# Performance work log

Hardware: AMD Instinct MI355X
Metric: run time of the kernel (lower is better)

Reference implementation:

```python
import jax, jax.numpy as jnp
import numpy as np

L, S = 3, 5                 # A hierarchy layers, subsets per layer
CIN = COUT = 64
INTER = COUT // (S - 1)     # 16
BC = COUT // 4              # 16 channels per TCN branch
N, T, V = 128, 128, 25
KS = 5
DILS = (1, 2)
EPS = 1e-5


def setup_inputs() -> dict:
    key = jax.random.key(0)
    ks = jax.random.split(key, 22)
    rn = lambda i, shape, s=0.1: jax.random.normal(ks[i], shape, jnp.float32) * s
    g1 = lambda i, shape: 1.0 + jax.random.normal(ks[i], shape, jnp.float32) * 0.05
    return {
        'x':      jax.random.normal(ks[0], (N, CIN, T, V), jnp.float32),
        'PA':     rn(1, (L, S, V, V), 0.2),
        'gdw':    rn(2, (L, INTER, CIN)),
        'gdb':    rn(3, (L, INTER)),
        'gdg':    g1(4, (L, INTER)),
        'gdbt':   rn(5, (L, INTER)),
        'gsw':    rn(6, (L, S, INTER, INTER)),
        'gsb':    rn(7, (L, S, INTER)),
        'gsg':    g1(8, (L, S, INTER)),
        'gsbt':   rn(9, (L, S, INTER)),
        'gbng':   g1(10, (COUT,)),
        'gbnb':   rn(11, (COUT,)),
        'brw':    rn(12, (4, BC, COUT)),
        'brb':    rn(13, (4, BC)),
        'brg':    g1(14, (4, BC)),
        'brbt':   rn(15, (4, BC)),
        'tcw':    rn(16, (2, BC, BC, KS, 1)),
        'tcbias': rn(17, (2, BC)),
        'tcg':    g1(18, (2, BC)),
        'tcbt':   rn(19, (2, BC)),
        'mpg':    g1(20, (BC,)),
        'mpb':    rn(21, (BC,)),
    }


def _bn(x, g, b):
    # training-mode BatchNorm2d over (N, T, V) with biased variance
    m = x.mean(axis=(0, 2, 3), keepdims=True)
    v = ((x - m) ** 2).mean(axis=(0, 2, 3), keepdims=True)
    return (x - m) * jax.lax.rsqrt(v + EPS) * g[None, :, None, None] + b[None, :, None, None]


def _c1x1(x, w, b=None):
    y = jnp.einsum('nctv,oc->notv', x, w)
    return y if b is None else y + b[None, :, None, None]


def reference(x, PA, gdw, gdb, gdg, gdbt, gsw, gsb, gsg, gsbt, gbng, gbnb,
              brw, brb, brg, brbt, tcw, tcbias, tcg, tcbt, mpg, mpb):
    # ---- UbH_Gconv ----
    layer_outs = []
    for i in range(L):
        xd = jax.nn.relu(_bn(_c1x1(x, gdw[i], gdb[i]), gdg[i], gdbt[i]))
        ys = [
            _bn(_c1x1(jnp.einsum('nctu,vu->nctv', xd, PA[i, j]), gsw[i, j], gsb[i, j]),
                gsg[i, j], gsbt[i, j])
            for j in range(S)
        ]
        layer_outs.append(jnp.concatenate(ys, axis=1))      # [N, S*INTER, T, V]
    out = jnp.stack(layer_outs, axis=2)                     # [N, S*INTER, L, T, V]
    base = out[:, :INTER]                                   # subset-0 block
    new = out[:, INTER:] + jnp.tile(base, (1, S - 1, 1, 1, 1))
    new = new.sum(axis=2)                                   # sum over hierarchy layers -> [N, COUT, T, V]
    xg = jax.nn.relu(_bn(new, gbng, gbnb) + x)              # residual down is identity (CIN==COUT)

    # ---- MultiScale_TemporalConv (residual=False) ----
    branches = []
    for k, d in enumerate(DILS):
        y = jax.nn.relu(_bn(_c1x1(xg, brw[k], brb[k]), brg[k], brbt[k]))
        pad = (KS + (KS - 1) * (d - 1) - 1) // 2
        y = jax.lax.conv_general_dilated(
            y, tcw[k], window_strides=(1, 1), padding=((pad, pad), (0, 0)),
            rhs_dilation=(d, 1), dimension_numbers=('NCHW', 'OIHW', 'NCHW'))
        y = y + tcbias[k][None, :, None, None]
        branches.append(_bn(y, tcg[k], tcbt[k]))
    # maxpool branch
    y = jax.nn.relu(_bn(_c1x1(xg, brw[2], brb[2]), brg[2], brbt[2]))
    y = jax.lax.reduce_window(y, -jnp.inf, jax.lax.max, (1, 1, 3, 1), (1, 1, 1, 1),
                              ((0, 0), (0, 0), (1, 1), (0, 0)))
    branches.append(_bn(y, mpg, mpb))
    # plain 1x1 branch
    branches.append(_bn(_c1x1(xg, brw[3], brb[3]), brg[3], brbt[3]))

    t = jnp.concatenate(branches, axis=1)                   # [N, COUT, T, V]
    # unit residual is identity (CIN==COUT, stride==1)
    return jax.nn.relu(t + xg)
```

## Files before the change

### kernel.cpp

```cpp
#include <hip/hip_runtime.h>

#define N_ 128
#define T_ 128
#define V_ 25
#define TV 3200
#define LL 3
#define SS 5
#define II 16
#define EPSB 1e-5f
#define MCNT 409600.0f


__device__ __forceinline__ float2 bncoef(const float2* st, int slot, float g, float bt){
  float2 s = st[slot];
  float m  = s.x * (1.0f/MCNT);
  float var = s.y * (1.0f/MCNT) - m*m;
  float a = g * rsqrtf(var + EPSB);
  return make_float2(a, bt - m*a);
}

__global__ __launch_bounds__(256) void k1_conv_dw(
    const float* __restrict__ x, const float* __restrict__ gdw, const float* __restrict__ gdb,
    float* __restrict__ c1, float2* st)
{
  __shared__ float w[64*48];
  __shared__ float bias[48];
  __shared__ float bst[4][96];
  const int tid = threadIdx.x;
  for (int i = tid; i < 64*48; i += 256){ int c = i/48, o = i - c*48; w[i] = gdw[o*64 + c]; }
  if (tid < 48) bias[tid] = gdb[tid];
  __syncthreads();
  const int n = blockIdx.y;
  const int rem = blockIdx.x*256 + tid;
  const bool act = rem < TV;
  float acc[48];
  #pragma unroll
  for (int o = 0; o < 48; o++) acc[o] = act ? bias[o] : 0.f;
  const float* xp = x + (size_t)n*64*TV + rem;
  if (act){
    #pragma unroll 4
    for (int c = 0; c < 64; c++){
      float xv = xp[c*TV];
      const float4* w4 = (const float4*)&w[c*48];
      #pragma unroll
      for (int o4 = 0; o4 < 12; o4++){
        float4 ww = w4[o4];
        acc[o4*4+0] += ww.x*xv; acc[o4*4+1] += ww.y*xv;
        acc[o4*4+2] += ww.z*xv; acc[o4*4+3] += ww.w*xv;
      }
    }
    #pragma unroll
    for (int o = 0; o < 48; o++){
      int l = o >> 4, oi = o & 15;
      c1[(size_t)((l*N_+n)*II + oi)*TV + rem] = acc[o];
    }
  }
  const int wv = tid >> 6, lane = tid & 63;
  #pragma unroll
  for (int o = 0; o < 48; o++){
    float s = acc[o], q = acc[o]*acc[o];
    #pragma unroll
    for (int m = 32; m; m >>= 1){ s += __shfl_xor(s, m); q += __shfl_xor(q, m); }
    if (lane == 0){ bst[wv][2*o] = s; bst[wv][2*o+1] = q; }
  }
  __syncthreads();
  float* stf = (float*)st;
  if (tid < 96) unsafeAtomicAdd(stf + tid, bst[0][tid]+bst[1][tid]+bst[2][tid]+bst[3][tid]);
}

__global__ __launch_bounds__(256) void k2_spatial_stats(
    const float* __restrict__ c1, const float* __restrict__ PA,
    const float* __restrict__ gsw, const float* __restrict__ gsb,
    const float* __restrict__ gdg, const float* __restrict__ gdbt,
    float2* st)
{
  __shared__ float zz[4][25][16];
  __shared__ float bst[4][160];
  const int tid = threadIdx.x;
  const int l = blockIdx.z, n = blockIdx.y;
  const int wu = __builtin_amdgcn_readfirstlane(tid >> 6);
  const int lane = tid & 63;
  const int t2 = lane >> 4, oc = lane & 15;
  const int t = blockIdx.x*4 + t2;
  float cAr, cBr;
  {
    float2 s = st[l*16+oc];
    float m = s.x*(1.f/MCNT), var = s.y*(1.f/MCNT) - m*m;
    cAr = gdg[l*16+oc]*rsqrtf(var+EPSB);
    cBr = gdbt[l*16+oc] - m*cAr;
  }
  float xdr[25];
  {
    const float* c1p = c1 + ((size_t)((l*N_+n)*II + oc))*TV + t*25;
    #pragma unroll
    for (int u = 0; u < 25; u++) xdr[u] = fmaxf(cAr*c1p[u] + cBr, 0.f);
  }
  #pragma unroll 1
  for (int j = 0; j < 5; j++){
    const float* paJ = PA + (size_t)(l*5+j)*625;
    const float* gwp = gsw + ((size_t)((l*5+j)*16 + oc))*16;
    float gwr[16];
    #pragma unroll
    for (int c4 = 0; c4 < 4; c4++){
      float4 g4 = *(const float4*)(gwp + 4*c4);
      gwr[4*c4+0]=g4.x; gwr[4*c4+1]=g4.y; gwr[4*c4+2]=g4.z; gwr[4*c4+3]=g4.w;
    }
    const float bjo = gsb[(l*5+j)*16 + oc];
    float ssum = 0.f, sq = 0.f;
    #pragma unroll
    for (int i = 0; i < 7; i++){
      const int vreal = wu + 4*i;
      const int v = vreal < 25 ? vreal : 24;
      const float* par = paJ + v*25;
      float pan[25];
      #pragma unroll
      for (int u = 0; u < 25; u++) pan[u] = par[u];
      if (vreal < 25){
        float z0 = xdr[0]*pan[0], z1 = xdr[1]*pan[1], z2 = xdr[2]*pan[2], z3 = xdr[3]*pan[3];
        #pragma unroll
        for (int u = 4; u < 24; u += 4){
          z0 += xdr[u+0]*pan[u+0];
          z1 += xdr[u+1]*pan[u+1];
          z2 += xdr[u+2]*pan[u+2];
          z3 += xdr[u+3]*pan[u+3];
        }
        z0 += xdr[24]*pan[24];
        zz[t2][v][oc] = (z0+z1)+(z2+z3);
        const float4* zr = (const float4*)&zz[t2][v][0];
        float4 za = zr[0], zb = zr[1], zc = zr[2], zd = zr[3];
        float d0 = gwr[0]*za.x + gwr[1]*za.y + gwr[2]*za.z + gwr[3]*za.w;
        float d1 = gwr[4]*zb.x + gwr[5]*zb.y + gwr[6]*zb.z + gwr[7]*zb.w;
        float d2 = gwr[8]*zc.x + gwr[9]*zc.y + gwr[10]*zc.z + gwr[11]*zc.w;
        float d3 = gwr[12]*zd.x + gwr[13]*zd.y + gwr[14]*zd.z + gwr[15]*zd.w;
        float cv = bjo + ((d0+d1)+(d2+d3));
        ssum += cv; sq += cv*cv;
      }
    }
    ssum += __shfl_xor(ssum,16); ssum += __shfl_xor(ssum,32);
    sq   += __shfl_xor(sq,16);   sq   += __shfl_xor(sq,32);
    if (t2 == 0){ bst[wu][2*(j*16+oc)] = ssum; bst[wu][2*(j*16+oc)+1] = sq; }
  }
  __syncthreads();
  float* stf = (float*)st;
  for (int i = tid; i < 160; i += 256)
    unsafeAtomicAdd(stf + 96 + l*160 + i, bst[0][i]+bst[1][i]+bst[2][i]+bst[3][i]);
}

__global__ __launch_bounds__(256) void k3_new(
    const float* __restrict__ c1, const float* __restrict__ PA,
    const float* __restrict__ gsw, const float* __restrict__ gsb,
    const float* __restrict__ gdg, const float* __restrict__ gdbt,
    const float* __restrict__ gsg, const float* __restrict__ gsbt,
    float2* st, float* __restrict__ newb)
{
  __shared__ float zz[4][25][16];
  __shared__ float bst[4][128];
  const int tid = threadIdx.x;
  const int n = blockIdx.y;
  const int wu = __builtin_amdgcn_readfirstlane(tid >> 6);
  const int lane = tid & 63;
  const int t2 = lane >> 4, oc = lane & 15;
  const int t = blockIdx.x*4 + t2;
  float base[7], ac1[7], ac2[7], ac3[7], ac4[7];
  #pragma unroll
  for (int i = 0; i < 7; i++){ base[i]=0.f; ac1[i]=0.f; ac2[i]=0.f; ac3[i]=0.f; ac4[i]=0.f; }

  #pragma unroll 1
  for (int l = 0; l < 3; l++){
    float cAr, cBr;
    {
      float2 s = st[l*16+oc];
      float m = s.x*(1.f/MCNT), var = s.y*(1.f/MCNT) - m*m;
      cAr = gdg[l*16+oc]*rsqrtf(var+EPSB);
      cBr = gdbt[l*16+oc] - m*cAr;
    }
    float xdr[25];
    {
      const float* c1p = c1 + ((size_t)((l*N_+n)*II + oc))*TV + t*25;
      #pragma unroll
      for (int u = 0; u < 25; u++) xdr[u] = fmaxf(cAr*c1p[u] + cBr, 0.f);
    }
    #pragma unroll 1
    for (int j = 0; j < 5; j++){
      const float* paJ = PA + (size_t)(l*5+j)*625;
      const float* gwp = gsw + ((size_t)((l*5+j)*16 + oc))*16;
      float gwr[16];
      #pragma unroll
      for (int c4 = 0; c4 < 4; c4++){
        float4 g4 = *(const float4*)(gwp + 4*c4);
        gwr[4*c4+0]=g4.x; gwr[4*c4+1]=g4.y; gwr[4*c4+2]=g4.z; gwr[4*c4+3]=g4.w;
      }
      const float bjo = gsb[(l*5+j)*16 + oc];
      float a2, b2;
      {
        int slot = 48 + (l*5+j)*16 + oc;
        float2 s = st[slot];
        float m = s.x*(1.f/MCNT), var = s.y*(1.f/MCNT) - m*m;
        a2 = gsg[(l*5+j)*16+oc]*rsqrtf(var+EPSB);
        b2 = gsbt[(l*5+j)*16+oc] - m*a2;
      }
      float yb_[7];
      #pragma unroll
      for (int i = 0; i < 7; i++){
        const int vreal = wu + 4*i;
        const int v = vreal < 25 ? vreal : 24;
        const float* par = paJ + v*25;
        float pan[25];
        #pragma unroll
        for (int u = 0; u < 25; u++) pan[u] = par[u];
        yb_[i] = 0.f;
        if (vreal < 25){
          float z0 = xdr[0]*pan[0], z1 = xdr[1]*pan[1], z2 = xdr[2]*pan[2], z3 = xdr[3]*pan[3];
          #pragma unroll
          for (int u = 4; u < 24; u += 4){
            z0 += xdr[u+0]*pan[u+0];
            z1 += xdr[u+1]*pan[u+1];
            z2 += xdr[u+2]*pan[u+2];
            z3 += xdr[u+3]*pan[u+3];
          }
          z0 += xdr[24]*pan[24];
          zz[t2][v][oc] = (z0+z1)+(z2+z3);
          const float4* zr = (const float4*)&zz[t2][v][0];
          float4 za = zr[0], zb = zr[1], zc = zr[2], zd = zr[3];
          float d0 = gwr[0]*za.x + gwr[1]*za.y + gwr[2]*za.z + gwr[3]*za.w;
          float d1 = gwr[4]*zb.x + gwr[5]*zb.y + gwr[6]*zb.z + gwr[7]*zb.w;
          float d2 = gwr[8]*zc.x + gwr[9]*zc.y + gwr[10]*zc.z + gwr[11]*zc.w;
          float d3 = gwr[12]*zd.x + gwr[13]*zd.y + gwr[14]*zd.z + gwr[15]*zd.w;
          yb_[i] = a2*(bjo + ((d0+d1)+(d2+d3))) + b2;
        }
      }
      if (j == 0){
        #pragma unroll
        for (int i = 0; i < 7; i++) base[i] += yb_[i];
      } else if (j == 1){
        #pragma unroll
        for (int i = 0; i < 7; i++) ac1[i] += yb_[i];
      } else if (j == 2){
        #pragma unroll
        for (int i = 0; i < 7; i++) ac2[i] += yb_[i];
      } else if (j == 3){
        #pragma unroll
        for (int i = 0; i < 7; i++) ac3[i] += yb_[i];
      } else {
        #pragma unroll
        for (int i = 0; i < 7; i++) ac4[i] += yb_[i];
      }
    }
  }
  float* np = newb + (size_t)n*64*TV + t*25;
  float s0=0.f,q0=0.f,s1=0.f,q1=0.f,s2=0.f,q2=0.f,s3=0.f,q3=0.f;
  #pragma unroll
  for (int i = 0; i < 7; i++){
    const int v = wu + 4*i;
    if (v < 25){
      float v0 = ac1[i] + base[i];
      float v1 = ac2[i] + base[i];
      float v2 = ac3[i] + base[i];
      float v3 = ac4[i] + base[i];
      np[(0*16+oc)*TV + v] = v0;
      np[(1*16+oc)*TV + v] = v1;
      np[(2*16+oc)*TV + v] = v2;
      np[(3*16+oc)*TV + v] = v3;
      s0 += v0; q0 += v0*v0;
      s1 += v1; q1 += v1*v1;
      s2 += v2; q2 += v2*v2;
      s3 += v3; q3 += v3*v3;
    }
  }
  s0 += __shfl_xor(s0,16); s0 += __shfl_xor(s0,32);
  q0 += __shfl_xor(q0,16); q0 += __shfl_xor(q0,32);
  s1 += __shfl_xor(s1,16); s1 += __shfl_xor(s1,32);
  q1 += __shfl_xor(q1,16); q1 += __shfl_xor(q1,32);
  s2 += __shfl_xor(s2,16); s2 += __shfl_xor(s2,32);
  q2 += __shfl_xor(q2,16); q2 += __shfl_xor(q2,32);
  s3 += __shfl_xor(s3,16); s3 += __shfl_xor(s3,32);
  q3 += __shfl_xor(q3,16); q3 += __shfl_xor(q3,32);
  if (t2 == 0){
    bst[wu][2*(0*16+oc)] = s0; bst[wu][2*(0*16+oc)+1] = q0;
    bst[wu][2*(1*16+oc)] = s1; bst[wu][2*(1*16+oc)+1] = q1;
    bst[wu][2*(2*16+oc)] = s2; bst[wu][2*(2*16+oc)+1] = q2;
    bst[wu][2*(3*16+oc)] = s3; bst[wu][2*(3*16+oc)+1] = q3;
  }
  __syncthreads();
  float* stf = (float*)st;
  for (int i = tid; i < 128; i += 256)
    unsafeAtomicAdd(stf + 576 + i, bst[0][i]+bst[1][i]+bst[2][i]+bst[3][i]);
}

__global__ __launch_bounds__(256) void k4_xg_branches(
    const float* __restrict__ x, const float* __restrict__ newb,
    const float* __restrict__ gbng, const float* __restrict__ gbnb,
    const float* __restrict__ brw, const float* __restrict__ brb,
    float2* st, float* __restrict__ xg, float* __restrict__ y)
{
  __shared__ float w[64*64];
  __shared__ float cA[64], cB[64], bias[64];
  __shared__ float bst[4][128];
  const int tid = threadIdx.x;
  for (int i = tid; i < 4096; i += 256){ int c = i >> 6, ko = i & 63; w[i] = brw[ko*64 + c]; }
  if (tid < 64){
    float2 ab = bncoef(st, 288+tid, gbng[tid], gbnb[tid]);
    cA[tid] = ab.x; cB[tid] = ab.y; bias[tid] = brb[tid];
  }
  __syncthreads();
  const int n = blockIdx.y;
  const int rem = blockIdx.x*256 + tid;
  const bool act = rem < TV;
  const float* xp  = x    + (size_t)n*64*TV + rem;
  const float* npx = newb + (size_t)n*64*TV + rem;
  float*       xgp = xg   + (size_t)n*64*TV + rem;
  float xgv[64];
  #pragma unroll
  for (int c = 0; c < 64; c++){
    float v = 0.f;
    if (act){
      v = fmaxf(cA[c]*npx[c*TV] + cB[c] + xp[c*TV], 0.f);
      xgp[c*TV] = v;
    }
    xgv[c] = v;
  }
  const int wv = tid >> 6, lane = tid & 63;
  #pragma unroll
  for (int k = 0; k < 4; k++){
    float acc[16];
    #pragma unroll
    for (int o = 0; o < 16; o++) acc[o] = act ? bias[k*16+o] : 0.f;
    #pragma unroll
    for (int c = 0; c < 64; c++){
      float xv = xgv[c];
      const float4* w4 = (const float4*)&w[c*64 + k*16];
      #pragma unroll
      for (int o4 = 0; o4 < 4; o4++){
        float4 ww = w4[o4];
        acc[o4*4+0] += ww.x*xv; acc[o4*4+1] += ww.y*xv;
        acc[o4*4+2] += ww.z*xv; acc[o4*4+3] += ww.w*xv;
      }
    }
    if (act){
      float* yp = y + (size_t)((k*N_+n)*16)*TV + rem;
      #pragma unroll
      for (int o = 0; o < 16; o++) yp[o*TV] = acc[o];
    }
    #pragma unroll
    for (int o = 0; o < 16; o++){
      float s = acc[o], q = acc[o]*acc[o];
      #pragma unroll
      for (int m = 32; m; m >>= 1){ s += __shfl_xor(s, m); q += __shfl_xor(q, m); }
      if (lane == 0){ bst[wv][2*(k*16+o)] = s; bst[wv][2*(k*16+o)+1] = q; }
    }
  }
  __syncthreads();
  float* stf = (float*)st;
  for (int i = tid; i < 128; i += 256)
    unsafeAtomicAdd(stf + 704 + i, bst[0][i]+bst[1][i]+bst[2][i]+bst[3][i]);
}

__global__ __launch_bounds__(256) void k5_temporal(
    const float* __restrict__ y, const float* __restrict__ tcw, const float* __restrict__ tcbias,
    const float* __restrict__ brg, const float* __restrict__ brbt,
    float2* st, float* __restrict__ tp)
{
  __shared__ float wt[2*16*5*16];
  __shared__ float cAy[48], cBy[48];
  __shared__ float bst[4][96];
  const int tid = threadIdx.x;
  for (int i = tid; i < 2560; i += 256){
    int k = i/1280, r = i - k*1280, c = r/80, r2 = r - c*80, ks = r2 >> 4, o = r2 & 15;
    wt[i] = tcw[((k*16+o)*16 + c)*5 + ks];
  }
  if (tid < 48){
    float2 ab = bncoef(st, 352+tid, brg[tid], brbt[tid]);
    cAy[tid] = ab.x; cBy[tid] = ab.y;
  }
  __syncthreads();
  const int n = blockIdx.y;
  const int rem = blockIdx.x*256 + tid;
  const bool act = rem < TV;
  const int t = rem/25, v = rem - t*25;
  const int wv = tid >> 6, lane = tid & 63;
  #pragma unroll
  for (int k = 0; k < 2; k++){
    const int d = k + 1;
    float acc[16];
    #pragma unroll
    for (int o = 0; o < 16; o++) acc[o] = act ? tcbias[k*16+o] : 0.f;
    if (act){
      const float* yp = y + (size_t)((k*N_+n)*16)*TV;
      #pragma unroll
      for (int ks = 0; ks < 5; ks++){
        int ttt = t + d*(ks-2);
        if (ttt >= 0 && ttt < T_){
          int off = ttt*25 + v;
          #pragma unroll
          for (int c = 0; c < 16; c++){
            float val = fmaxf(cAy[k*16+c]*yp[c*TV + off] + cBy[k*16+c], 0.f);
            const float4* w4 = (const float4*)&wt[((k*16+c)*5 + ks)*16];
            #pragma unroll
            for (int o4 = 0; o4 < 4; o4++){
              float4 ww = w4[o4];
              acc[o4*4+0] += ww.x*val; acc[o4*4+1] += ww.y*val;
              acc[o4*4+2] += ww.z*val; acc[o4*4+3] += ww.w*val;
            }
          }
        }
      }
      float* op = tp + (size_t)k*6553600 + (size_t)(n*16)*TV + rem;
      #pragma unroll
      for (int o = 0; o < 16; o++) op[o*TV] = acc[o];
    }
    #pragma unroll
    for (int o = 0; o < 16; o++){
      float s = acc[o], q = acc[o]*acc[o];
      #pragma unroll
      for (int m = 32; m; m >>= 1){ s += __shfl_xor(s, m); q += __shfl_xor(q, m); }
      if (lane == 0){ bst[wv][2*(k*16+o)] = s; bst[wv][2*(k*16+o)+1] = q; }
    }
  }
  {
    float mx[16];
    #pragma unroll
    for (int o = 0; o < 16; o++) mx[o] = -1e30f;
    if (act){
      const float* yp = y + (size_t)((2*N_+n)*16)*TV;
      #pragma unroll
      for (int dt = -1; dt <= 1; dt++){
        int ttt = t + dt;
        if (ttt >= 0 && ttt < T_){
          int off = ttt*25 + v;
          #pragma unroll
          for (int o = 0; o < 16; o++){
            float val = fmaxf(cAy[32+o]*yp[o*TV + off] + cBy[32+o], 0.f);
            mx[o] = fmaxf(mx[o], val);
          }
        }
      }
      float* op = tp + (size_t)2*6553600 + (size_t)(n*16)*TV + rem;
      #pragma unroll
      for (int o = 0; o < 16; o++) op[o*TV] = mx[o];
    } else {
      #pragma unroll
      for (int o = 0; o < 16; o++) mx[o] = 0.f;
    }
    #pragma unroll
    for (int o = 0; o < 16; o++){
      float s = mx[o], q = mx[o]*mx[o];
      #pragma unroll
      for (int m = 32; m; m >>= 1){ s += __shfl_xor(s, m); q += __shfl_xor(q, m); }
      if (lane == 0){ bst[wv][64 + 2*o] = s; bst[wv][64 + 2*o + 1] = q; }
    }
  }
  __syncthreads();
  float* stf = (float*)st;
  for (int i = tid; i < 96; i += 256)
    unsafeAtomicAdd(stf + 832 + i, bst[0][i]+bst[1][i]+bst[2][i]+bst[3][i]);
}

__global__ __launch_bounds__(256) void k6_final(
    const float* __restrict__ tp, const float* __restrict__ y, const float* __restrict__ xg,
    const float* __restrict__ tcg, const float* __restrict__ tcbt,
    const float* __restrict__ mpg, const float* __restrict__ mpb,
    const float* __restrict__ brg, const float* __restrict__ brbt,
    const float2* __restrict__ st, float* __restrict__ out)
{
  __shared__ float cA[64], cB[64];
  const int tid = threadIdx.x;
  if (tid < 64){
    int o = tid & 15;
    float2 ab;
    if (tid < 32)      ab = bncoef(st, 416 + tid, tcg[tid], tcbt[tid]);
    else if (tid < 48) ab = bncoef(st, 448 + o, mpg[o], mpb[o]);
    else               ab = bncoef(st, 400 + o, brg[48+o], brbt[48+o]);
    cA[tid] = ab.x; cB[tid] = ab.y;
  }
  __syncthreads();
  const int n = blockIdx.y;
  const int rem = blockIdx.x*256 + tid;
  if (rem >= TV) return;
  const float* xgp = xg + (size_t)n*64*TV + rem;
  float* op = out + (size_t)n*64*TV + rem;
  #pragma unroll
  for (int ch = 0; ch < 64; ch++){
    int o = ch & 15;
    float sv;
    if (ch < 48) sv = tp[(size_t)(ch>>4)*6553600 + (size_t)(n*16+o)*TV + rem];
    else         sv = y[(size_t)((3*N_+n)*16 + o)*TV + rem];
    float val = cA[ch]*sv + cB[ch] + xgp[ch*TV];
    op[ch*TV] = fmaxf(val, 0.f);
  }
}

extern "C" void kernel_launch(void* const* d_in, const int* in_sizes, int n_in,
                              void* d_out, int out_size, void* d_ws, size_t ws_size,
                              hipStream_t stream) {
  (void)in_sizes; (void)n_in; (void)out_size; (void)ws_size;
  const float* x    = (const float*)d_in[0];
  const float* PA   = (const float*)d_in[1];
  const float* gdw  = (const float*)d_in[2];
  const float* gdb  = (const float*)d_in[3];
  const float* gdg  = (const float*)d_in[4];
  const float* gdbt = (const float*)d_in[5];
  const float* gsw  = (const float*)d_in[6];
  const float* gsb  = (const float*)d_in[7];
  const float* gsg  = (const float*)d_in[8];
  const float* gsbt = (const float*)d_in[9];
  const float* gbng = (const float*)d_in[10];
  const float* gbnb = (const float*)d_in[11];
  const float* brw  = (const float*)d_in[12];
  const float* brb  = (const float*)d_in[13];
  const float* brg  = (const float*)d_in[14];
  const float* brbt = (const float*)d_in[15];
  const float* tcw  = (const float*)d_in[16];
  const float* tcbias=(const float*)d_in[17];
  const float* tcg  = (const float*)d_in[18];
  const float* tcbt = (const float*)d_in[19];
  const float* mpg  = (const float*)d_in[20];
  const float* mpb  = (const float*)d_in[21];

  char* ws = (char*)d_ws;
  float2* st  = (float2*)ws;
  float* c1   = (float*)(ws + 4096);
  float* tp   = c1;
  float* newb = (float*)(ws + 4096 + 78643200);
  float* xg   = (float*)(ws + 4096 + 78643200 + 104857600);
  float* y    = (float*)(ws + 4096 + 78643200 + 209715200);

  hipMemsetAsync(st, 0, 4096, stream);
  dim3 b(256);
  k1_conv_dw     <<<dim3(13,128),   b, 0, stream>>>(x, gdw, gdb, c1, st);
  k2_spatial_stats<<<dim3(32,128,3), b, 0, stream>>>(c1, PA, gsw, gsb, gdg, gdbt, st);
  k3_new         <<<dim3(32,128),   b, 0, stream>>>(c1, PA, gsw, gsb, gdg, gdbt, gsg, gsbt, st, newb);
  k4_xg_branches <<<dim3(13,128),   b, 0, stream>>>(x, newb, gbng, gbnb, brw, brb, st, xg, y);
  k5_temporal    <<<dim3(13,128),   b, 0, stream>>>(y, tcw, tcbias, brg, brbt, st, tp);
  k6_final       <<<dim3(13,128),   b, 0, stream>>>(tp, y, xg, tcg, tcbt, mpg, mpb, brg, brbt, st, (float*)d_out);
}
```

Before: 1.420 ms.

## Materialize spatial conv outputs in k2 and read them in k3 instead of recomputing

The spatial graph-conv stage computes the per-subset outputs twice: once to gather BN statistics and again to build the merged hierarchy features. When the workspace is large enough, k2 now writes all 15 subset outputs (about 393 MB) and a new k3_read kernel only applies the BN affine and accumulates, avoiding a second pass of the PA and gsw matmuls. This trades recomputation for a large extra write and read of global memory. If the workspace is too small, the old recompute path is kept. Both kernels also split the z computation and the channel mixing into separate loops, and the shared base accumulator is folded into the four partial sums.

```diff
diff --git a/kernel.cpp b/kernel.cpp
--- a/kernel.cpp
+++ b/kernel.cpp
@@ -68,11 +68,11 @@
   if (tid < 96) unsafeAtomicAdd(stf + tid, bst[0][tid]+bst[1][tid]+bst[2][tid]+bst[3][tid]);
 }
 
-__global__ __launch_bounds__(256) void k2_spatial_stats(
+__global__ __launch_bounds__(256) void k2_spatial(
     const float* __restrict__ c1, const float* __restrict__ PA,
     const float* __restrict__ gsw, const float* __restrict__ gsb,
     const float* __restrict__ gdg, const float* __restrict__ gdbt,
-    float2* st)
+    float2* st, float* __restrict__ c2out, const int storec2)
 {
   __shared__ float zz[4][25][16];
   __shared__ float bst[4][160];
@@ -106,7 +106,6 @@
       gwr[4*c4+0]=g4.x; gwr[4*c4+1]=g4.y; gwr[4*c4+2]=g4.z; gwr[4*c4+3]=g4.w;
     }
     const float bjo = gsb[(l*5+j)*16 + oc];
-    float ssum = 0.f, sq = 0.f;
     #pragma unroll
     for (int i = 0; i < 7; i++){
       const int vreal = wu + 4*i;
@@ -126,7 +125,14 @@
         }
         z0 += xdr[24]*pan[24];
         zz[t2][v][oc] = (z0+z1)+(z2+z3);
-        const float4* zr = (const float4*)&zz[t2][v][0];
+      }
+    }
+    float ssum = 0.f, sq = 0.f;
+    #pragma unroll
+    for (int i = 0; i < 7; i++){
+      const int vreal = wu + 4*i;
+      if (vreal < 25){
+        const float4* zr = (const float4*)&zz[t2][vreal][0];
         float4 za = zr[0], zb = zr[1], zc = zr[2], zd = zr[3];
         float d0 = gwr[0]*za.x + gwr[1]*za.y + gwr[2]*za.z + gwr[3]*za.w;
         float d1 = gwr[4]*zb.x + gwr[5]*zb.y + gwr[6]*zb.z + gwr[7]*zb.w;
@@ -134,6 +140,9 @@
         float d3 = gwr[12]*zd.x + gwr[13]*zd.y + gwr[14]*zd.z + gwr[15]*zd.w;
         float cv = bjo + ((d0+d1)+(d2+d3));
         ssum += cv; sq += cv*cv;
+        if (storec2){
+          c2out[((((size_t)(l*5+j)*N_ + n)*25 + vreal)*T_ + t)*16 + oc] = cv;
+        }
       }
     }
     ssum += __shfl_xor(ssum,16); ssum += __shfl_xor(ssum,32);
@@ -144,6 +153,101 @@
   float* stf = (float*)st;
   for (int i = tid; i < 160; i += 256)
     unsafeAtomicAdd(stf + 96 + l*160 + i, bst[0][i]+bst[1][i]+bst[2][i]+bst[3][i]);
+}
+
+__global__ __launch_bounds__(256) void k3_read(
+    const float* __restrict__ c2, const float* __restrict__ gsg, const float* __restrict__ gsbt,
+    float2* st, float* __restrict__ newb)
+{
+  __shared__ float cofA[15][16], cofB[15][16];
+  __shared__ float bst[4][128];
+  const int tid = threadIdx.x;
+  const int n = blockIdx.y;
+  if (tid < 240){
+    int lj = tid >> 4, o = tid & 15;
+    float2 s = st[48 + lj*16 + o];
+    float m = s.x*(1.f/MCNT), var = s.y*(1.f/MCNT) - m*m;
+    float a = gsg[lj*16+o]*rsqrtf(var+EPSB);
+    cofA[lj][o] = a; cofB[lj][o] = gsbt[lj*16+o] - m*a;
+  }
+  __syncthreads();
+  const int wu = __builtin_amdgcn_readfirstlane(tid >> 6);
+  const int lane = tid & 63;
+  const int t2 = lane >> 4, oc = lane & 15;
+  const int t = blockIdx.x*4 + t2;
+  float ac1[7], ac2[7], ac3[7], ac4[7];
+  #pragma unroll
+  for (int i = 0; i < 7; i++){ ac1[i]=0.f; ac2[i]=0.f; ac3[i]=0.f; ac4[i]=0.f; }
+  #pragma unroll 1
+  for (int l = 0; l < 3; l++){
+    #pragma unroll 1
+    for (int j = 0; j < 5; j++){
+      const int lj = l*5 + j;
+      const float a2 = cofA[lj][oc], b2 = cofB[lj][oc];
+      const float* cp = c2 + (((size_t)lj*N_ + n)*25)*T_*16 + (size_t)t*16 + oc;
+      float yb_[7];
+      #pragma unroll
+      for (int i = 0; i < 7; i++){
+        const int vreal = wu + 4*i;
+        yb_[i] = 0.f;
+        if (vreal < 25){
+          float cv = cp[(size_t)vreal*T_*16];
+          yb_[i] = a2*cv + b2;
+        }
+      }
+      if (j == 0){
+        #pragma unroll
+        for (int i = 0; i < 7; i++){ ac1[i]+=yb_[i]; ac2[i]+=yb_[i]; ac3[i]+=yb_[i]; ac4[i]+=yb_[i]; }
+      } else if (j == 1){
+        #pragma unroll
+        for (int i = 0; i < 7; i++) ac1[i] += yb_[i];
+      } else if (j == 2){
+        #pragma unroll
+        for (int i = 0; i < 7; i++) ac2[i] += yb_[i];
+      } else if (j == 3){
+        #pragma unroll
+        for (int i = 0; i < 7; i++) ac3[i] += yb_[i];
+      } else {
+        #pragma unroll
+        for (int i = 0; i < 7; i++) ac4[i] += yb_[i];
+      }
+    }
+  }
+  float* np = newb + (size_t)n*64*TV + t*25;
+  float s0=0.f,q0=0.f,s1=0.f,q1=0.f,s2=0.f,q2=0.f,s3=0.f,q3=0.f;
+  #pragma unroll
+  for (int i = 0; i < 7; i++){
+    const int v = wu + 4*i;
+    if (v < 25){
+      float v0 = ac1[i], v1 = ac2[i], v2 = ac3[i], v3 = ac4[i];
+      np[(0*16+oc)*TV + v] = v0;
+      np[(1*16+oc)*TV + v] = v1;
+      np[(2*16+oc)*TV + v] = v2;
+      np[(3*16+oc)*TV + v] = v3;
+      s0 += v0; q0 += v0*v0;
+      s1 += v1; q1 += v1*v1;
+      s2 += v2; q2 += v2*v2;
+      s3 += v3; q3 += v3*v3;
+    }
+  }
+  s0 += __shfl_xor(s0,16); s0 += __shfl_xor(s0,32);
+  q0 += __shfl_xor(q0,16); q0 += __shfl_xor(q0,32);
+  s1 += __shfl_xor(s1,16); s1 += __shfl_xor(s1,32);
+  q1 += __shfl_xor(q1,16); q1 += __shfl_xor(q1,32);
+  s2 += __shfl_xor(s2,16); s2 += __shfl_xor(s2,32);
+  q2 += __shfl_xor(q2,16); q2 += __shfl_xor(q2,32);
+  s3 += __shfl_xor(s3,16); s3 += __shfl_xor(s3,32);
+  q3 += __shfl_xor(q3,16); q3 += __shfl_xor(q3,32);
+  if (t2 == 0){
+    bst[wu][2*(0*16+oc)] = s0; bst[wu][2*(0*16+oc)+1] = q0;
+    bst[wu][2*(1*16+oc)] = s1; bst[wu][2*(1*16+oc)+1] = q1;
+    bst[wu][2*(2*16+oc)] = s2; bst[wu][2*(2*16+oc)+1] = q2;
+    bst[wu][2*(3*16+oc)] = s3; bst[wu][2*(3*16+oc)+1] = q3;
+  }
+  __syncthreads();
+  float* stf = (float*)st;
+  for (int i = tid; i < 128; i += 256)
+    unsafeAtomicAdd(stf + 576 + i, bst[0][i]+bst[1][i]+bst[2][i]+bst[3][i]);
 }
 
 __global__ __launch_bounds__(256) void k3_new(
@@ -161,9 +265,9 @@
   const int lane = tid & 63;
   const int t2 = lane >> 4, oc = lane & 15;
   const int t = blockIdx.x*4 + t2;
-  float base[7], ac1[7], ac2[7], ac3[7], ac4[7];
-  #pragma unroll
-  for (int i = 0; i < 7; i++){ base[i]=0.f; ac1[i]=0.f; ac2[i]=0.f; ac3[i]=0.f; ac4[i]=0.f; }
+  float ac1[7], ac2[7], ac3[7], ac4[7];
+  #pragma unroll
+  for (int i = 0; i < 7; i++){ ac1[i]=0.f; ac2[i]=0.f; ac3[i]=0.f; ac4[i]=0.f; }
 
   #pragma unroll 1
   for (int l = 0; l < 3; l++){
@@ -199,7 +303,6 @@
         a2 = gsg[(l*5+j)*16+oc]*rsqrtf(var+EPSB);
         b2 = gsbt[(l*5+j)*16+oc] - m*a2;
       }
-      float yb_[7];
       #pragma unroll
       for (int i = 0; i < 7; i++){
         const int vreal = wu + 4*i;
@@ -208,7 +311,6 @@
         float pan[25];
         #pragma unroll
         for (int u = 0; u < 25; u++) pan[u] = par[u];
-        yb_[i] = 0.f;
         if (vreal < 25){
           float z0 = xdr[0]*pan[0], z1 = xdr[1]*pan[1], z2 = xdr[2]*pan[2], z3 = xdr[3]*pan[3];
           #pragma unroll
@@ -220,7 +322,15 @@
           }
           z0 += xdr[24]*pan[24];
           zz[t2][v][oc] = (z0+z1)+(z2+z3);
-          const float4* zr = (const float4*)&zz[t2][v][0];
+        }
+      }
+      float yb_[7];
+      #pragma unroll
+      for (int i = 0; i < 7; i++){
+        const int vreal = wu + 4*i;
+        yb_[i] = 0.f;
+        if (vreal < 25){
+          const float4* zr = (const float4*)&zz[t2][vreal][0];
           float4 za = zr[0], zb = zr[1], zc = zr[2], zd = zr[3];
           float d0 = gwr[0]*za.x + gwr[1]*za.y + gwr[2]*za.z + gwr[3]*za.w;
           float d1 = gwr[4]*zb.x + gwr[5]*zb.y + gwr[6]*zb.z + gwr[7]*zb.w;
@@ -231,7 +341,7 @@
       }
       if (j == 0){
         #pragma unroll
-        for (int i = 0; i < 7; i++) base[i] += yb_[i];
+        for (int i = 0; i < 7; i++){ ac1[i]+=yb_[i]; ac2[i]+=yb_[i]; ac3[i]+=yb_[i]; ac4[i]+=yb_[i]; }
       } else if (j == 1){
         #pragma unroll
         for (int i = 0; i < 7; i++) ac1[i] += yb_[i];
@@ -253,10 +363,7 @@
   for (int i = 0; i < 7; i++){
     const int v = wu + 4*i;
     if (v < 25){
-      float v0 = ac1[i] + base[i];
-      float v1 = ac2[i] + base[i];
-      float v2 = ac3[i] + base[i];
-      float v3 = ac4[i] + base[i];
+      float v0 = ac1[i], v1 = ac2[i], v2 = ac3[i], v3 = ac4[i];
       np[(0*16+oc)*TV + v] = v0;
       np[(1*16+oc)*TV + v] = v1;
       np[(2*16+oc)*TV + v] = v2;
@@ -492,7 +599,7 @@
 extern "C" void kernel_launch(void* const* d_in, const int* in_sizes, int n_in,
                               void* d_out, int out_size, void* d_ws, size_t ws_size,
                               hipStream_t stream) {
-  (void)in_sizes; (void)n_in; (void)out_size; (void)ws_size;
+  (void)in_sizes; (void)n_in; (void)out_size;
   const float* x    = (const float*)d_in[0];
   const float* PA   = (const float*)d_in[1];
   const float* gdw  = (const float*)d_in[2];
@@ -517,19 +624,38 @@
   const float* mpb  = (const float*)d_in[21];
 
   char* ws = (char*)d_ws;
+  const size_t OFF_C1   = 4096;
+  const size_t SZ_C1    = 78643200ull;
+  const size_t SZ_C2    = 393216000ull;
+  const size_t SZ_MAP   = 104857600ull;
+  const size_t NEED_BIG = OFF_C1 + SZ_C1 + SZ_C2 + 3*SZ_MAP;
+
+  const bool big = ws_size >= NEED_BIG;
+
   float2* st  = (float2*)ws;
-  float* c1   = (float*)(ws + 4096);
+  float* c1   = (float*)(ws + OFF_C1);
   float* tp   = c1;
-  float* newb = (float*)(ws + 4096 + 78643200);
-  float* xg   = (float*)(ws + 4096 + 78643200 + 104857600);
-  float* y    = (float*)(ws + 4096 + 78643200 + 209715200);
+  float* c2   = (float*)(ws + OFF_C1 + SZ_C1);
+  float* newb, *xg, *y;
+  if (big){
+    newb = (float*)(ws + OFF_C1 + SZ_C1 + SZ_C2);
+    xg   = (float*)(ws + OFF_C1 + SZ_C1 + SZ_C2 + SZ_MAP);
+    y    = (float*)(ws + OFF_C1 + SZ_C1 + SZ_C2 + 2*SZ_MAP);
+  } else {
+    newb = (float*)(ws + OFF_C1 + SZ_C1);
+    xg   = (float*)(ws + OFF_C1 + SZ_C1 + SZ_MAP);
+    y    = (float*)(ws + OFF_C1 + SZ_C1 + 2*SZ_MAP);
+  }
 
   hipMemsetAsync(st, 0, 4096, stream);
   dim3 b(256);
-  k1_conv_dw     <<<dim3(13,128),   b, 0, stream>>>(x, gdw, gdb, c1, st);
-  k2_spatial_stats<<<dim3(32,128,3), b, 0, stream>>>(c1, PA, gsw, gsb, gdg, gdbt, st);
-  k3_new         <<<dim3(32,128),   b, 0, stream>>>(c1, PA, gsw, gsb, gdg, gdbt, gsg, gsbt, st, newb);
-  k4_xg_branches <<<dim3(13,128),   b, 0, stream>>>(x, newb, gbng, gbnb, brw, brb, st, xg, y);
-  k5_temporal    <<<dim3(13,128),   b, 0, stream>>>(y, tcw, tcbias, brg, brbt, st, tp);
-  k6_final       <<<dim3(13,128),   b, 0, stream>>>(tp, y, xg, tcg, tcbt, mpg, mpb, brg, brbt, st, (float*)d_out);
-}
+  k1_conv_dw   <<<dim3(13,128),   b, 0, stream>>>(x, gdw, gdb, c1, st);
+  k2_spatial   <<<dim3(32,128,3), b, 0, stream>>>(c1, PA, gsw, gsb, gdg, gdbt, st, c2, big ? 1 : 0);
+  if (big)
+    k3_read    <<<dim3(32,128),   b, 0, stream>>>(c2, gsg, gsbt, st, newb);
+  else
+    k3_new     <<<dim3(32,128),   b, 0, stream>>>(c1, PA, gsw, gsb, gdg, gdbt, gsg, gsbt, st, newb);
+  k4_xg_branches<<<dim3(13,128),  b, 0, stream>>>(x, newb, gbng, gbnb, brw, brb, st, xg, y);
+  k5_temporal  <<<dim3(13,128),   b, 0, stream>>>(y, tcw, tcbias, brg, brbt, st, tp);
+  k6_final     <<<dim3(13,128),   b, 0, stream>>>(tp, y, xg, tcg, tcbt, mpg, mpb, brg, brbt, st, (float*)d_out);
+}
```

Measured after the change: 1.307 ms. 1.09x faster.
